# Kernel tuning notes

Hardware: AMD Instinct MI355X
Metric: run time of the kernel (lower is better)

## Reference

```python
import jax, jax.numpy as jnp
import numpy as np

B, DIM, S = 8, 512, 1024
H, DH = 8, 64
FF_INNER = 1024      # dim * (ff_mult//2)
CONV_INNER = 1024    # dim * expansion_factor
K = 31
PAD = (K - 1) // 2


def _bn(x, g, b):
    # eval-mode BatchNorm2d with running stats (0,1) absorbed: per-channel affine
    return x * g[None, :, None, None] + b[None, :, None, None]


def _pw(x, w, b):
    # 1x1 Conv2d == channel matmul. x: [B,C,S,1], w: [O,C]
    return jnp.einsum('oc,bcst->bost', w, x) + b[None, :, None, None]


def _ff(x, g, b, w1, b1, w2, b2):
    h = _pw(_bn(x, g, b), w1, b1)
    return _pw(jax.nn.silu(h), w2, b2)


def _attn(x, g, b, wq, bq, wk, bk, wv, bv, wo, bo):
    xn = _bn(x, g, b)
    q = _pw(xn, wq, bq)[..., 0].reshape(B, H, DH, S)
    k = _pw(xn, wk, bk)[..., 0].reshape(B, H, DH, S)
    v = _pw(xn, wv, bv)[..., 0].reshape(B, H, DH, S)
    scale = DH ** -0.5
    scores = jnp.einsum('bhds,bhdt->bhst', q, k) * scale   # [B,H,S,S]
    w = jax.nn.softmax(scores, axis=-1)
    o = jnp.einsum('bhst,bhdt->bhds', w, v).reshape(B, H * DH, S)[..., None]
    return _pw(o, wo, bo)


def _conv(x, g, b, pw1_w, pw1_b, dconv_w, dconv_b, cbn_g, cbn_b, pw2_w, pw2_b):
    h = _pw(_bn(x, g, b), pw1_w, pw1_b)          # [B,2*CONV_INNER,S,1]
    a, gate = jnp.split(h, 2, axis=1)
    h = a * jax.nn.sigmoid(gate)                  # GLU
    h = jnp.transpose(h, (0, 1, 3, 2))            # [B,C,1,S] so kernel (1,K) runs along seq
    h = jax.lax.conv_general_dilated(
        h, dconv_w, window_strides=(1, 1), padding=((0, 0), (PAD, PAD)),
        dimension_numbers=('NCHW', 'OIHW', 'NCHW'))
    h = jnp.transpose(h, (0, 1, 3, 2)) + dconv_b[None, :, None, None]
    h = jax.nn.silu(_bn(h, cbn_g, cbn_b))
    return _pw(h, pw2_w, pw2_b)


def setup_inputs() -> dict:
    key = jax.random.key(0)
    ks = iter(jax.random.split(key, 32))
    w = lambda *s: jax.random.normal(next(ks), s, jnp.float32) * 0.02
    d = {
        'x': jax.random.normal(next(ks), (B, DIM, S, 1), jnp.float32),
        'ff1_g': jnp.ones((DIM,)), 'ff1_b': jnp.zeros((DIM,)),
        'ff1_w1': w(FF_INNER, DIM), 'ff1_b1': jnp.zeros((FF_INNER,)),
        'ff1_w2': w(DIM, FF_INNER), 'ff1_b2': jnp.zeros((DIM,)),
        'attn_g': jnp.ones((DIM,)), 'attn_b': jnp.zeros((DIM,)),
        'wq': w(H * DH, DIM), 'bq': jnp.zeros((H * DH,)),
        'wk': w(H * DH, DIM), 'bk': jnp.zeros((H * DH,)),
        'wv': w(H * DH, DIM), 'bv': jnp.zeros((H * DH,)),
        'wo': w(DIM, H * DH), 'bo': jnp.zeros((DIM,)),
        'conv_g': jnp.ones((DIM,)), 'conv_b': jnp.zeros((DIM,)),
        'pw1_w': w(2 * CONV_INNER, DIM), 'pw1_b': jnp.zeros((2 * CONV_INNER,)),
        'dconv_w': w(CONV_INNER, CONV_INNER, 1, K), 'dconv_b': jnp.zeros((CONV_INNER,)),
        'cbn_g': jnp.ones((CONV_INNER,)), 'cbn_b': jnp.zeros((CONV_INNER,)),
        'pw2_w': w(DIM, CONV_INNER), 'pw2_b': jnp.zeros((DIM,)),
        'ff2_g': jnp.ones((DIM,)), 'ff2_b': jnp.zeros((DIM,)),
        'ff2_w1': w(FF_INNER, DIM), 'ff2_b1': jnp.zeros((FF_INNER,)),
        'ff2_w2': w(DIM, FF_INNER), 'ff2_b2': jnp.zeros((DIM,)),
        'fin_g': jnp.ones((DIM,)), 'fin_b': jnp.zeros((DIM,)),
    }
    return d


def reference(x, ff1_g, ff1_b, ff1_w1, ff1_b1, ff1_w2, ff1_b2,
              attn_g, attn_b, wq, bq, wk, bk, wv, bv, wo, bo,
              conv_g, conv_b, pw1_w, pw1_b, dconv_w, dconv_b, cbn_g, cbn_b, pw2_w, pw2_b,
              ff2_g, ff2_b, ff2_w1, ff2_b1, ff2_w2, ff2_b2, fin_g, fin_b):
    x1 = x + 0.5 * _ff(x, ff1_g, ff1_b, ff1_w1, ff1_b1, ff1_w2, ff1_b2)
    x2 = x1 + _attn(x1, attn_g, attn_b, wq, bq, wk, bk, wv, bv, wo, bo)
    x3 = x2 + _conv(x2, conv_g, conv_b, pw1_w, pw1_b, dconv_w, dconv_b, cbn_g, cbn_b, pw2_w, pw2_b)
    x4 = x3 + 0.5 * _ff(x3, ff2_g, ff2_b, ff2_w1, ff2_b1, ff2_w2, ff2_b2)
    return _bn(x4, fin_g, fin_b)
```

## Files before the change

### kernel.cpp

```cpp
#include <hip/hip_runtime.h>
#include <cstdint>
#include <cstddef>

using bf16 = __bf16;
typedef __bf16 bf16x8 __attribute__((ext_vector_type(8)));
typedef float f32x4 __attribute__((ext_vector_type(4)));
typedef unsigned int uint4v __attribute__((ext_vector_type(4)));

#define NB 8
#define DIM 512
#define SEQ 1024
#define NH 8
#define DH 64
#define CONV_INNER 1024
#define KW 31
#define PADW 15
#define HPRA 1056

__device__ __forceinline__ float fsigmoid(float x) { return 1.f / (1.f + __expf(-x)); }
__device__ __forceinline__ float fsilu(float x) { return x * fsigmoid(x); }

__device__ __forceinline__ void gld16(const bf16* g, bf16* l) {
  __builtin_amdgcn_global_load_lds(
      (const __attribute__((address_space(1))) unsigned int*)g,
      (__attribute__((address_space(3))) unsigned int*)l, 16, 0, 0);
}


__global__ __launch_bounds__(256) void k_diag(float* __restrict__ out, int n, float v) {
  int i = blockIdx.x * 256 + threadIdx.x;
  if (i < n) out[i] = v;
}


__global__ __launch_bounds__(256) void k_convert_bf16(const float* __restrict__ src,
                                                      bf16* __restrict__ dst, int n) {
  int i = (blockIdx.x * 256 + threadIdx.x) * 4;
  if (i + 3 < n) {
    float4 v = *reinterpret_cast<const float4*>(src + i);
    dst[i]     = (bf16)v.x;
    dst[i + 1] = (bf16)v.y;
    dst[i + 2] = (bf16)v.z;
    dst[i + 3] = (bf16)v.w;
  }
}

__global__ __launch_bounds__(256) void k_conv_wt(const float* __restrict__ w,
                                                 bf16* __restrict__ wt) {
  __shared__ float t[256 * KW];
  int o = blockIdx.x, i0 = blockIdx.y * 256;
  const float* src = w + (size_t)o * (CONV_INNER * KW) + (size_t)i0 * KW;
  for (int idx = threadIdx.x; idx < 256 * KW; idx += 256) t[idx] = src[idx];
  __syncthreads();
  for (int k = 0; k < KW; ++k) {
    wt[((size_t)k * CONV_INNER + o) * CONV_INNER + i0 + threadIdx.x] =
        (bf16)t[threadIdx.x * KW + k];
  }
}

__global__ __launch_bounds__(256) void k_pad_zero(bf16* __restrict__ hpad) {
  int i = blockIdx.x * 256 + threadIdx.x;
  int b = i / (32 * 128);
  int r = (i >> 7) & 31;
  int c8 = (i & 127) * 8;
  int row = (r < PADW) ? r : 1024 + r;
  uint4v z = {0u, 0u, 0u, 0u};
  *reinterpret_cast<uint4v*>(&hpad[((size_t)b * HPRA + row) * CONV_INNER + c8]) = z;
}

__global__ __launch_bounds__(256) void k_transpose_in(const float* __restrict__ x,
                                                      const float* __restrict__ g,
                                                      const float* __restrict__ bvec,
                                                      float* __restrict__ xT,
                                                      bf16* __restrict__ xbn) {
  __shared__ float t[32][33];
  int s0 = blockIdx.x * 32, c0 = blockIdx.y * 32, b = blockIdx.z;
  int col = threadIdx.x & 31, rq = threadIdx.x >> 5;
#pragma unroll
  for (int i = 0; i < 4; ++i) {
    int row = rq + i * 8;
    t[row][col] = x[((size_t)b * DIM + c0 + row) * SEQ + s0 + col];
  }
  __syncthreads();
  float gg = g[c0 + col], bb = bvec[c0 + col];
#pragma unroll
  for (int i = 0; i < 4; ++i) {
    int srow = rq + i * 8;
    float v = t[col][srow];
    size_t off = ((size_t)b * SEQ + s0 + srow) * DIM + c0 + col;
    xT[off] = v;
    xbn[off] = (bf16)(v * gg + bb);
  }
}

__global__ __launch_bounds__(256) void k_concat_bias(const float* __restrict__ bq,
                                                     const float* __restrict__ bk,
                                                     const float* __restrict__ bv,
                                                     float* __restrict__ qb) {
  int i = blockIdx.x * 256 + threadIdx.x;
  if (i < 512) qb[i] = bq[i];
  else if (i < 1024) qb[i] = bk[i - 512];
  else if (i < 1536) qb[i] = bv[i - 1024];
}

template <int EPI>
__global__ __launch_bounds__(256) void k_gemm(const bf16* __restrict__ A,
                                              const bf16* __restrict__ W,
                                              const float* __restrict__ bias,
                                              const float* __restrict__ res,
                                              const float* __restrict__ g,
                                              const float* __restrict__ bb,
                                              float* __restrict__ outf,
                                              bf16* __restrict__ outb, int N, int K) {
  __shared__ __align__(16) bf16 sA[128][40];
  __shared__ __align__(16) bf16 sB[128][40];
  const int tid = threadIdx.x;
  const int b = blockIdx.z;
  const int m0 = blockIdx.y * 128, n0 = blockIdx.x * 128;
  const int lane = tid & 63, wid = tid >> 6;
  const int wm = (wid & 1) * 64, wn = (wid >> 1) * 64;
  const int fr = lane & 15, fg = lane >> 4;

  f32x4 acc[4][4];
#pragma unroll
  for (int i = 0; i < 4; ++i)
#pragma unroll
    for (int j = 0; j < 4; ++j) acc[i][j] = (f32x4)0.f;

  const int srow = tid >> 1, sc = (tid & 1) * 16;
  const bf16* Abase = A + ((size_t)b * SEQ + m0 + srow) * K + sc;
  const bf16* Wbase = W + (size_t)(n0 + srow) * K + sc;

  for (int kt = 0; kt < K; kt += 32) {
    uint4v a0 = *reinterpret_cast<const uint4v*>(Abase + kt);
    uint4v a1 = *reinterpret_cast<const uint4v*>(Abase + kt + 8);
    uint4v w0 = *reinterpret_cast<const uint4v*>(Wbase + kt);
    uint4v w1 = *reinterpret_cast<const uint4v*>(Wbase + kt + 8);
    *reinterpret_cast<uint4v*>(&sA[srow][sc]) = a0;
    *reinterpret_cast<uint4v*>(&sA[srow][sc + 8]) = a1;
    *reinterpret_cast<uint4v*>(&sB[srow][sc]) = w0;
    *reinterpret_cast<uint4v*>(&sB[srow][sc + 8]) = w1;
    __syncthreads();
    bf16x8 aF[4], bF[4];
#pragma unroll
    for (int i = 0; i < 4; ++i) {
      aF[i] = *reinterpret_cast<const bf16x8*>(&sA[wm + i * 16 + fr][fg * 8]);
      bF[i] = *reinterpret_cast<const bf16x8*>(&sB[wn + i * 16 + fr][fg * 8]);
    }
#pragma unroll
    for (int mi = 0; mi < 4; ++mi)
#pragma unroll
      for (int ni = 0; ni < 4; ++ni)
        acc[mi][ni] =
            __builtin_amdgcn_mfma_f32_16x16x32_bf16(aF[mi], bF[ni], acc[mi][ni], 0, 0, 0);
    __syncthreads();
  }

#pragma unroll
  for (int mi = 0; mi < 4; ++mi) {
#pragma unroll
    for (int ni = 0; ni < 4; ++ni) {
      int ncol = n0 + wn + ni * 16 + fr;
      float bv = bias[ncol];
      if constexpr (EPI == 5) {
        float gg = g[ncol], bbv = bb[ncol];
        int mrow0 = m0 + wm + mi * 16 + fg * 4;
        float v[4];
#pragma unroll
        for (int j = 0; j < 4; ++j) {
          float a = acc[mi][ni][j] + bv;
          float r = res[((size_t)b * SEQ + mrow0 + j) * 512 + ncol] + 0.5f * a;
          v[j] = r * gg + bbv;
        }
        *reinterpret_cast<float4*>(outf + ((size_t)b * 512 + ncol) * SEQ + mrow0) =
            make_float4(v[0], v[1], v[2], v[3]);
      } else {
#pragma unroll
        for (int j = 0; j < 4; ++j) {
          int mrow = m0 + wm + mi * 16 + fg * 4 + j;
          size_t off = ((size_t)b * SEQ + mrow) * N + ncol;
          float a = acc[mi][ni][j] + bv;
          if constexpr (EPI == 0) {
            outb[off] = (bf16)fsilu(a);
          } else if constexpr (EPI == 2) {
            outb[off] = (bf16)a;
          } else if constexpr (EPI == 1) {
            float r = res[off] + 0.5f * a;
            outf[off] = r;
            outb[off] = (bf16)(r * g[ncol] + bb[ncol]);
          } else if constexpr (EPI == 3) {
            float r = res[off] + a;
            outf[off] = r;
            outb[off] = (bf16)(r * g[ncol] + bb[ncol]);
          }
        }
      }
    }
  }
}

__global__ __launch_bounds__(256) void k_pw1_glu(const bf16* __restrict__ A,
                                                 const bf16* __restrict__ W,
                                                 const float* __restrict__ bias,
                                                 bf16* __restrict__ hpad) {
  __shared__ __align__(16) bf16 sA[128][40];
  __shared__ __align__(16) bf16 sBa[128][40];
  __shared__ __align__(16) bf16 sBg[128][40];
  const int tid = threadIdx.x;
  const int b = blockIdx.z;
  const int m0 = blockIdx.y * 128, n0 = blockIdx.x * 128;
  const int lane = tid & 63, wid = tid >> 6;
  const int wm = (wid & 1) * 64, wn = (wid >> 1) * 64;
  const int fr = lane & 15, fg = lane >> 4;
  const int K = 512;

  f32x4 accA[4][4], accG[4][4];
#pragma unroll
  for (int i = 0; i < 4; ++i)
#pragma unroll
    for (int j = 0; j < 4; ++j) { accA[i][j] = (f32x4)0.f; accG[i][j] = (f32x4)0.f; }

  const int srow = tid >> 1, sc = (tid & 1) * 16;
  const bf16* Abase = A + ((size_t)b * SEQ + m0 + srow) * K + sc;
  const bf16* WaB = W + (size_t)(n0 + srow) * K + sc;
  const bf16* WgB = W + (size_t)(n0 + 1024 + srow) * K + sc;

  for (int kt = 0; kt < K; kt += 32) {
    uint4v a0 = *reinterpret_cast<const uint4v*>(Abase + kt);
    uint4v a1 = *reinterpret_cast<const uint4v*>(Abase + kt + 8);
    uint4v wa0 = *reinterpret_cast<const uint4v*>(WaB + kt);
    uint4v wa1 = *reinterpret_cast<const uint4v*>(WaB + kt + 8);
    uint4v wg0 = *reinterpret_cast<const uint4v*>(WgB + kt);
    uint4v wg1 = *reinterpret_cast<const uint4v*>(WgB + kt + 8);
    *reinterpret_cast<uint4v*>(&sA[srow][sc]) = a0;
    *reinterpret_cast<uint4v*>(&sA[srow][sc + 8]) = a1;
    *reinterpret_cast<uint4v*>(&sBa[srow][sc]) = wa0;
    *reinterpret_cast<uint4v*>(&sBa[srow][sc + 8]) = wa1;
    *reinterpret_cast<uint4v*>(&sBg[srow][sc]) = wg0;
    *reinterpret_cast<uint4v*>(&sBg[srow][sc + 8]) = wg1;
    __syncthreads();
    bf16x8 aF[4], bFa[4], bFg[4];
#pragma unroll
    for (int i = 0; i < 4; ++i) {
      aF[i]  = *reinterpret_cast<const bf16x8*>(&sA[wm + i * 16 + fr][fg * 8]);
      bFa[i] = *reinterpret_cast<const bf16x8*>(&sBa[wn + i * 16 + fr][fg * 8]);
      bFg[i] = *reinterpret_cast<const bf16x8*>(&sBg[wn + i * 16 + fr][fg * 8]);
    }
#pragma unroll
    for (int mi = 0; mi < 4; ++mi)
#pragma unroll
      for (int ni = 0; ni < 4; ++ni) {
        accA[mi][ni] =
            __builtin_amdgcn_mfma_f32_16x16x32_bf16(aF[mi], bFa[ni], accA[mi][ni], 0, 0, 0);
        accG[mi][ni] =
            __builtin_amdgcn_mfma_f32_16x16x32_bf16(aF[mi], bFg[ni], accG[mi][ni], 0, 0, 0);
      }
    __syncthreads();
  }

#pragma unroll
  for (int mi = 0; mi < 4; ++mi) {
#pragma unroll
    for (int ni = 0; ni < 4; ++ni) {
      int ncol = n0 + wn + ni * 16 + fr;
      float ba = bias[ncol], bg = bias[ncol + 1024];
#pragma unroll
      for (int j = 0; j < 4; ++j) {
        int mrow = m0 + wm + mi * 16 + fg * 4 + j;
        float av = accA[mi][ni][j] + ba;
        float gv = accG[mi][ni][j] + bg;
        hpad[((size_t)b * HPRA + PADW + mrow) * CONV_INNER + ncol] =
            (bf16)(av * fsigmoid(gv));
      }
    }
  }
}

__global__ __launch_bounds__(256) void k_conv(const bf16* __restrict__ hpad,
                                              const bf16* __restrict__ wt,
                                              const float* __restrict__ bias,
                                              const float* __restrict__ g,
                                              const float* __restrict__ bb,
                                              bf16* __restrict__ outb) {
  __shared__ __align__(16) bf16 sA[160 * 64];
  __shared__ __align__(16) bf16 sB0[128 * 64];
  __shared__ __align__(16) bf16 sB1[128 * 64];
  const int tid = threadIdx.x;
  const int b = blockIdx.z;
  const int n0 = blockIdx.x * 128, m0 = blockIdx.y * 128;
  const int lane = tid & 63, wid = tid >> 6;
  const int wm = (wid & 1) * 64, wn = (wid >> 1) * 64;
  const int fr = lane & 15, fg = lane >> 4;
  const int srow = lane >> 3;
  const int scol = ((lane & 7) ^ srow) * 8;

  f32x4 acc[4][4];
#pragma unroll
  for (int i = 0; i < 4; ++i)
#pragma unroll
    for (int j = 0; j < 4; ++j) acc[i][j] = (f32x4)0.f;

  const bf16* Abase = hpad + ((size_t)b * HPRA + m0 + srow) * CONV_INNER + scol;
  const bf16* Wbase = wt + (size_t)(n0 + srow) * CONV_INNER + scol;

  for (int it = 0; it < 16; ++it) {
    const int itc = it * 64;
#pragma unroll
    for (int c = 0; c < 5; ++c) {
      const int ch = wid + c * 4;
      gld16(Abase + (size_t)(ch * 8) * CONV_INNER + itc, &sA[ch * 512]);
    }
#pragma unroll
    for (int c = 0; c < 4; ++c) {
      const int ch = wid + c * 4;
      gld16(Wbase + (size_t)(ch * 8) * CONV_INNER + itc, &sB0[ch * 512]);
    }
    __syncthreads();

    for (int ks = 0; ks < KW; ++ks) {
      const bf16* cur = (ks & 1) ? sB1 : sB0;
      bf16* nxt = (ks & 1) ? sB0 : sB1;
      if (ks + 1 < KW) {
#pragma unroll
        for (int c = 0; c < 4; ++c) {
          const int ch = wid + c * 4;
          gld16(Wbase + (size_t)(ks + 1) * CONV_INNER * CONV_INNER +
                    (size_t)(ch * 8) * CONV_INNER + itc,
                &nxt[ch * 512]);
        }
      }
#pragma unroll
      for (int kk = 0; kk < 2; ++kk) {
        const int cg = kk * 4 + fg;
        bf16x8 aF[4], bF[4];
#pragma unroll
        for (int i = 0; i < 4; ++i) {
          const int ar = ks + wm + i * 16 + fr;
          aF[i] = *reinterpret_cast<const bf16x8*>(
              &sA[ar * 64 + ((cg ^ (ar & 7)) * 8)]);
        }
#pragma unroll
        for (int n = 0; n < 4; ++n) {
          const int br = wn + n * 16 + fr;
          bF[n] = *reinterpret_cast<const bf16x8*>(
              &cur[br * 64 + ((cg ^ (br & 7)) * 8)]);
        }
#pragma unroll
        for (int mi = 0; mi < 4; ++mi)
#pragma unroll
          for (int ni = 0; ni < 4; ++ni)
            acc[mi][ni] = __builtin_amdgcn_mfma_f32_16x16x32_bf16(aF[mi], bF[ni],
                                                                  acc[mi][ni], 0, 0, 0);
      }
      __syncthreads();
    }
  }

#pragma unroll
  for (int mi = 0; mi < 4; ++mi) {
#pragma unroll
    for (int ni = 0; ni < 4; ++ni) {
      int ncol = n0 + wn + ni * 16 + fr;
      float bv = bias[ncol], gg = g[ncol], bbv = bb[ncol];
#pragma unroll
      for (int j = 0; j < 4; ++j) {
        int mrow = m0 + wm + mi * 16 + fg * 4 + j;
        float a = acc[mi][ni][j] + bv;
        outb[((size_t)b * SEQ + mrow) * CONV_INNER + ncol] = (bf16)fsilu(a * gg + bbv);
      }
    }
  }
}

__global__ __launch_bounds__(256) void k_attn(const bf16* __restrict__ qkv,
                                              bf16* __restrict__ out) {
  __shared__ __align__(16) bf16 sQ[128][72];
  __shared__ __align__(16) bf16 sK[64][72];
  __shared__ __align__(16) bf16 sVT[64][72];
  __shared__ __align__(16) bf16 sP[128][72];
  const int tid = threadIdx.x;
  const int bh = blockIdx.y;
  const int b = bh >> 3, h = bh & 7;
  const int m0 = blockIdx.x * 128;
  const int lane = tid & 63, wid = tid >> 6;
  const int w32 = wid * 32;
  const int fr = lane & 15, fg = lane >> 4;
  const size_t base = (size_t)b * SEQ * 1536;

  for (int idx = tid; idx < 128 * 8; idx += 256) {
    int row = idx >> 3, c = (idx & 7) * 8;
    *reinterpret_cast<uint4v*>(&sQ[row][c]) =
        *reinterpret_cast<const uint4v*>(qkv + base + (size_t)(m0 + row) * 1536 + h * 64 + c);
  }

  f32x4 o[2][4];
  float mst[2][4], lst[2][4];
#pragma unroll
  for (int mi = 0; mi < 2; ++mi)
#pragma unroll
    for (int j = 0; j < 4; ++j) {
      mst[mi][j] = -1e30f;
      lst[mi][j] = 0.f;
#pragma unroll
      for (int df = 0; df < 4; ++df) o[mi][df] = (f32x4)0.f;
    }

  for (int t0 = 0; t0 < SEQ; t0 += 64) {
    for (int idx = tid; idx < 64 * 8; idx += 256) {
      int row = idx >> 3, c = (idx & 7) * 8;
      *reinterpret_cast<uint4v*>(&sK[row][c]) = *reinterpret_cast<const uint4v*>(
          qkv + base + (size_t)(t0 + row) * 1536 + 512 + h * 64 + c);
    }
    for (int e = tid; e < 64 * 64; e += 256) {
      int t = e >> 6, d = e & 63;
      sVT[d][t] = qkv[base + (size_t)(t0 + t) * 1536 + 1024 + h * 64 + d];
    }
    __syncthreads();

    f32x4 sacc[2][4];
#pragma unroll
    for (int mi = 0; mi < 2; ++mi)
#pragma unroll
      for (int tf = 0; tf < 4; ++tf) sacc[mi][tf] = (f32x4)0.f;
#pragma unroll
    for (int kk = 0; kk < 2; ++kk) {
      bf16x8 aQ[2], bK[4];
#pragma unroll
      for (int mi = 0; mi < 2; ++mi)
        aQ[mi] = *reinterpret_cast<const bf16x8*>(&sQ[w32 + mi * 16 + fr][kk * 32 + fg * 8]);
#pragma unroll
      for (int tf = 0; tf < 4; ++tf)
        bK[tf] = *reinterpret_cast<const bf16x8*>(&sK[tf * 16 + fr][kk * 32 + fg * 8]);
#pragma unroll
      for (int mi = 0; mi < 2; ++mi)
#pragma unroll
        for (int tf = 0; tf < 4; ++tf)
          sacc[mi][tf] =
              __builtin_amdgcn_mfma_f32_16x16x32_bf16(aQ[mi], bK[tf], sacc[mi][tf], 0, 0, 0);
    }

#pragma unroll
    for (int mi = 0; mi < 2; ++mi) {
#pragma unroll
      for (int j = 0; j < 4; ++j) {
        float rm = -1e30f;
#pragma unroll
        for (int tf = 0; tf < 4; ++tf) rm = fmaxf(rm, sacc[mi][tf][j] * 0.125f);
#pragma unroll
        for (int off = 1; off < 16; off <<= 1) rm = fmaxf(rm, __shfl_xor(rm, off));
        float mnew = fmaxf(mst[mi][j], rm);
        float al = __expf(mst[mi][j] - mnew);
        float ps = 0.f;
#pragma unroll
        for (int tf = 0; tf < 4; ++tf) {
          float p = __expf(sacc[mi][tf][j] * 0.125f - mnew);
          ps += p;
          sP[w32 + mi * 16 + fg * 4 + j][tf * 16 + fr] = (bf16)p;
        }
#pragma unroll
        for (int off = 1; off < 16; off <<= 1) ps += __shfl_xor(ps, off);
        lst[mi][j] = lst[mi][j] * al + ps;
        mst[mi][j] = mnew;
#pragma unroll
        for (int df = 0; df < 4; ++df) o[mi][df][j] *= al;
      }
    }
    __syncthreads();

#pragma unroll
    for (int kk = 0; kk < 2; ++kk) {
      bf16x8 aP[2], bV[4];
#pragma unroll
      for (int mi = 0; mi < 2; ++mi)
        aP[mi] = *reinterpret_cast<const bf16x8*>(&sP[w32 + mi * 16 + fr][kk * 32 + fg * 8]);
#pragma unroll
      for (int df = 0; df < 4; ++df)
        bV[df] = *reinterpret_cast<const bf16x8*>(&sVT[df * 16 + fr][kk * 32 + fg * 8]);
#pragma unroll
      for (int mi = 0; mi < 2; ++mi)
#pragma unroll
        for (int df = 0; df < 4; ++df)
          o[mi][df] = __builtin_amdgcn_mfma_f32_16x16x32_bf16(aP[mi], bV[df], o[mi][df], 0, 0, 0);
    }
    __syncthreads();
  }

#pragma unroll
  for (int mi = 0; mi < 2; ++mi)
#pragma unroll
    for (int df = 0; df < 4; ++df)
#pragma unroll
      for (int j = 0; j < 4; ++j) {
        int row = m0 + w32 + mi * 16 + fg * 4 + j;
        int col = h * 64 + df * 16 + fr;
        out[((size_t)b * SEQ + row) * 512 + col] = (bf16)(o[mi][df][j] / lst[mi][j]);
      }
}


extern "C" void kernel_launch(void* const* d_in, const int* in_sizes, int n_in,
                              void* d_out, int out_size, void* d_ws, size_t ws_size,
                              hipStream_t stream) {
  const float* x      = (const float*)d_in[0];
  const float* ff1_g  = (const float*)d_in[1];
  const float* ff1_b  = (const float*)d_in[2];
  const float* ff1_w1 = (const float*)d_in[3];
  const float* ff1_b1 = (const float*)d_in[4];
  const float* ff1_w2 = (const float*)d_in[5];
  const float* ff1_b2 = (const float*)d_in[6];
  const float* attn_g = (const float*)d_in[7];
  const float* attn_b = (const float*)d_in[8];
  const float* wq     = (const float*)d_in[9];
  const float* bq     = (const float*)d_in[10];
  const float* wk     = (const float*)d_in[11];
  const float* bk     = (const float*)d_in[12];
  const float* wv     = (const float*)d_in[13];
  const float* bv     = (const float*)d_in[14];
  const float* wo     = (const float*)d_in[15];
  const float* bo     = (const float*)d_in[16];
  const float* conv_g = (const float*)d_in[17];
  const float* conv_b = (const float*)d_in[18];
  const float* pw1_w  = (const float*)d_in[19];
  const float* pw1_b  = (const float*)d_in[20];
  const float* dconv_w = (const float*)d_in[21];
  const float* dconv_b = (const float*)d_in[22];
  const float* cbn_g  = (const float*)d_in[23];
  const float* cbn_b  = (const float*)d_in[24];
  const float* pw2_w  = (const float*)d_in[25];
  const float* pw2_b  = (const float*)d_in[26];
  const float* ff2_g  = (const float*)d_in[27];
  const float* ff2_b  = (const float*)d_in[28];
  const float* ff2_w1 = (const float*)d_in[29];
  const float* ff2_b1 = (const float*)d_in[30];
  const float* ff2_w2 = (const float*)d_in[31];
  const float* ff2_b2 = (const float*)d_in[32];
  const float* fin_g  = (const float*)d_in[33];
  const float* fin_b  = (const float*)d_in[34];

  char* ws = (char*)d_ws;
  size_t off = 0;
  auto alloc = [&](size_t bytes) -> void* {
    off = (off + 255) & ~(size_t)255;
    void* p = ws + off;
    off += bytes;
    return p;
  };

  bf16* wqkv  = (bf16*)alloc((size_t)1536 * 512 * 2);
  float* qkvb = (float*)alloc(1536 * 4);
  bf16* wf1a  = (bf16*)alloc((size_t)1024 * 512 * 2);
  bf16* wf1b  = (bf16*)alloc((size_t)512 * 1024 * 2);
  bf16* wwo   = (bf16*)alloc((size_t)512 * 512 * 2);
  bf16* wpw1  = (bf16*)alloc((size_t)2048 * 512 * 2);
  bf16* wpw2  = (bf16*)alloc((size_t)512 * 1024 * 2);
  bf16* wf2a  = (bf16*)alloc((size_t)1024 * 512 * 2);
  bf16* wf2b  = (bf16*)alloc((size_t)512 * 1024 * 2);

  bf16*  Bn  = (bf16*)alloc((size_t)NB * SEQ * 512 * 2);
  float* F1  = (float*)alloc((size_t)NB * SEQ * 512 * 4);
  bf16*  HGp = (bf16*)alloc((size_t)NB * HPRA * 1024 * 2);
  bf16*  H2  = (bf16*)alloc((size_t)NB * SEQ * 1024 * 2);

  char* E = (char*)alloc((size_t)KW * 1024 * 1024 * 2);
  bf16*  wt     = (bf16*)E;
  bf16*  h1     = (bf16*)E;
  bf16*  qkv    = (bf16*)E;
  bf16*  attn_o = (bf16*)(E + (size_t)24 * 1024 * 1024);
  float* x1     = (float*)(E + (size_t)32 * 1024 * 1024);
  float* x3     = (float*)E;
  bf16*  h3     = (bf16*)(E + (size_t)16 * 1024 * 1024);

  float* xT = F1;
  float* x2 = F1;
  bf16* xbn = Bn, *x1bn = Bn, *x2bn = Bn, *x3bn = Bn;
  size_t needed = off;
  (void)in_sizes; (void)n_in;

  if (ws_size < needed) {
    k_diag<<<(out_size + 255) / 256, 256, 0, stream>>>(
        (float*)d_out, out_size, (float)(ws_size >> 20));
    return;
  }

  auto cvt = [&](const float* s, bf16* d, int n) {
    k_convert_bf16<<<n / 1024, 256, 0, stream>>>(s, d, n);
  };
  cvt(wq, wqkv, 512 * 512);
  cvt(wk, wqkv + 512 * 512, 512 * 512);
  cvt(wv, wqkv + 1024 * 512, 512 * 512);
  cvt(ff1_w1, wf1a, 1024 * 512);
  cvt(ff1_w2, wf1b, 512 * 1024);
  cvt(wo, wwo, 512 * 512);
  cvt(pw1_w, wpw1, 2048 * 512);
  cvt(pw2_w, wpw2, 512 * 1024);
  cvt(ff2_w1, wf2a, 1024 * 512);
  cvt(ff2_w2, wf2b, 512 * 1024);
  k_concat_bias<<<6, 256, 0, stream>>>(bq, bk, bv, qkvb);
  k_pad_zero<<<(NB * 32 * 128) / 256, 256, 0, stream>>>(HGp);
  k_transpose_in<<<dim3(32, 16, NB), 256, 0, stream>>>(x, ff1_g, ff1_b, xT, xbn);

  k_gemm<0><<<dim3(8, 8, NB), 256, 0, stream>>>(xbn, wf1a, ff1_b1, nullptr, nullptr,
                                                nullptr, nullptr, h1, 1024, 512);
  k_gemm<1><<<dim3(4, 8, NB), 256, 0, stream>>>(h1, wf1b, ff1_b2, xT, attn_g, attn_b,
                                                x1, x1bn, 512, 1024);
  k_gemm<2><<<dim3(12, 8, NB), 256, 0, stream>>>(x1bn, wqkv, qkvb, nullptr, nullptr,
                                                 nullptr, nullptr, qkv, 1536, 512);
  k_attn<<<dim3(8, 64), 256, 0, stream>>>(qkv, attn_o);
  k_gemm<3><<<dim3(4, 8, NB), 256, 0, stream>>>(attn_o, wwo, bo, x1, conv_g, conv_b,
                                                x2, x2bn, 512, 512);
  k_conv_wt<<<dim3(1024, 4), 256, 0, stream>>>(dconv_w, wt);
  k_pw1_glu<<<dim3(8, 8, NB), 256, 0, stream>>>(x2bn, wpw1, pw1_b, HGp);
  k_conv<<<dim3(8, 8, NB), 256, 0, stream>>>(HGp, wt, dconv_b, cbn_g, cbn_b, H2);
  k_gemm<3><<<dim3(4, 8, NB), 256, 0, stream>>>(H2, wpw2, pw2_b, x2, ff2_g, ff2_b,
                                                x3, x3bn, 512, 1024);
  k_gemm<0><<<dim3(8, 8, NB), 256, 0, stream>>>(x3bn, wf2a, ff2_b1, nullptr, nullptr,
                                                nullptr, nullptr, h3, 1024, 512);
  k_gemm<5><<<dim3(4, 8, NB), 256, 0, stream>>>(h3, wf2b, ff2_b2, x3, fin_g, fin_b,
                                                (float*)d_out, nullptr, 512, 1024);
}
```

Baseline: 818.3 us.

## Double-buffer GEMM K-tiles via direct global-to-LDS loads with XOR swizzle

The shared GEMM kernel now stages 64-wide K tiles into two LDS buffers using global_load_lds, prefetching the next tile while MFMAs run on the current one. The LDS layout is XOR-swizzled to avoid bank conflicts on fragment reads, replacing the padded 32-wide layout. This cuts one barrier per iteration and the register round-trip for loads. It raises LDS use to 64 KB per block, which may lower occupancy, and it relies on gld16 completing before the single barrier.

```diff
diff --git a/kernel.cpp b/kernel.cpp
--- a/kernel.cpp
+++ b/kernel.cpp
@@ -112,14 +112,16 @@
                                               const float* __restrict__ bb,
                                               float* __restrict__ outf,
                                               bf16* __restrict__ outb, int N, int K) {
-  __shared__ __align__(16) bf16 sA[128][40];
-  __shared__ __align__(16) bf16 sB[128][40];
+  __shared__ __align__(16) bf16 sA[2][128 * 64];
+  __shared__ __align__(16) bf16 sB[2][128 * 64];
   const int tid = threadIdx.x;
   const int b = blockIdx.z;
   const int m0 = blockIdx.y * 128, n0 = blockIdx.x * 128;
   const int lane = tid & 63, wid = tid >> 6;
   const int wm = (wid & 1) * 64, wn = (wid >> 1) * 64;
   const int fr = lane & 15, fg = lane >> 4;
+  const int srow = lane >> 3;
+  const int scol = ((lane & 7) ^ srow) * 8;
 
   f32x4 acc[4][4];
 #pragma unroll
@@ -127,33 +129,51 @@
 #pragma unroll
     for (int j = 0; j < 4; ++j) acc[i][j] = (f32x4)0.f;
 
-  const int srow = tid >> 1, sc = (tid & 1) * 16;
-  const bf16* Abase = A + ((size_t)b * SEQ + m0 + srow) * K + sc;
-  const bf16* Wbase = W + (size_t)(n0 + srow) * K + sc;
-
-  for (int kt = 0; kt < K; kt += 32) {
-    uint4v a0 = *reinterpret_cast<const uint4v*>(Abase + kt);
-    uint4v a1 = *reinterpret_cast<const uint4v*>(Abase + kt + 8);
-    uint4v w0 = *reinterpret_cast<const uint4v*>(Wbase + kt);
-    uint4v w1 = *reinterpret_cast<const uint4v*>(Wbase + kt + 8);
-    *reinterpret_cast<uint4v*>(&sA[srow][sc]) = a0;
-    *reinterpret_cast<uint4v*>(&sA[srow][sc + 8]) = a1;
-    *reinterpret_cast<uint4v*>(&sB[srow][sc]) = w0;
-    *reinterpret_cast<uint4v*>(&sB[srow][sc + 8]) = w1;
+  const bf16* Abase = A + ((size_t)b * SEQ + m0 + srow) * K + scol;
+  const bf16* Wbase = W + (size_t)(n0 + srow) * K + scol;
+  const int nch = K >> 6;
+
+#pragma unroll
+  for (int c = 0; c < 4; ++c) {
+    const int ch = wid + c * 4;
+    gld16(Abase + (size_t)(ch * 8) * K, &sA[0][ch * 512]);
+    gld16(Wbase + (size_t)(ch * 8) * K, &sB[0][ch * 512]);
+  }
+  __syncthreads();
+
+  int buf = 0;
+  for (int kt = 0; kt < nch; ++kt) {
+    if (kt + 1 < nch) {
+      const int kc = (kt + 1) * 64;
+#pragma unroll
+      for (int c = 0; c < 4; ++c) {
+        const int ch = wid + c * 4;
+        gld16(Abase + (size_t)(ch * 8) * K + kc, &sA[buf ^ 1][ch * 512]);
+        gld16(Wbase + (size_t)(ch * 8) * K + kc, &sB[buf ^ 1][ch * 512]);
+      }
+    }
+#pragma unroll
+    for (int kk = 0; kk < 2; ++kk) {
+      const int cg = kk * 4 + fg;
+      bf16x8 aF[4], bF[4];
+#pragma unroll
+      for (int i = 0; i < 4; ++i) {
+        const int ar = wm + i * 16 + fr;
+        aF[i] = *reinterpret_cast<const bf16x8*>(
+            &sA[buf][ar * 64 + ((cg ^ (ar & 7)) * 8)]);
+        const int br = wn + i * 16 + fr;
+        bF[i] = *reinterpret_cast<const bf16x8*>(
+            &sB[buf][br * 64 + ((cg ^ (br & 7)) * 8)]);
+      }
+#pragma unroll
+      for (int mi = 0; mi < 4; ++mi)
+#pragma unroll
+        for (int ni = 0; ni < 4; ++ni)
+          acc[mi][ni] = __builtin_amdgcn_mfma_f32_16x16x32_bf16(aF[mi], bF[ni],
+                                                                acc[mi][ni], 0, 0, 0);
+    }
     __syncthreads();
-    bf16x8 aF[4], bF[4];
-#pragma unroll
-    for (int i = 0; i < 4; ++i) {
-      aF[i] = *reinterpret_cast<const bf16x8*>(&sA[wm + i * 16 + fr][fg * 8]);
-      bF[i] = *reinterpret_cast<const bf16x8*>(&sB[wn + i * 16 + fr][fg * 8]);
-    }
-#pragma unroll
-    for (int mi = 0; mi < 4; ++mi)
-#pragma unroll
-      for (int ni = 0; ni < 4; ++ni)
-        acc[mi][ni] =
-            __builtin_amdgcn_mfma_f32_16x16x32_bf16(aF[mi], bF[ni], acc[mi][ni], 0, 0, 0);
-    __syncthreads();
+    buf ^= 1;
   }
 
 #pragma unroll
```

After: 786.0 us. 1.04x faster.
